# Performance work log

Hardware: AMD Instinct MI355X
Metric: run time of the kernel (lower is better)

## Reference

```python
import jax, jax.numpy as jnp
import numpy as np
from math import ceil, log2

LEVELS = 6
N = 4096
DB4 = np.array([0.23037781330885523, 0.7148465705525415, 0.6308807679295904,
                -0.02798376941698385, -0.18703481171888114, 0.030841381835986965,
                0.032883011666982945, -0.010597401784997278], dtype=np.float32)


def setup_inputs() -> dict:
    key = jax.random.key(0)
    x = jax.random.normal(key, (N, N), dtype=jnp.float32)
    # learned filter bank: scaling.repeat(levels*2, 1)
    scaling = jnp.tile(jnp.asarray(DB4), (LEVELS * 2, 1))
    return {
        "x": x,
        "scaling": scaling,
        "alpha": jnp.float32(10.0),
        "b_plus": jnp.float32(2.0),
        "b_minus": jnp.float32(1.0),
    }


def compute_wavelet(h):
    # g_k = flip(h); odd indices negated
    g = jnp.flip(h, -1)
    sign = jnp.where(jnp.arange(g.shape[-1]) % 2 == 1, -1.0, 1.0).astype(g.dtype)
    return g * sign


def convolve(x, f, transpose=False):
    # circular convolution (or correlation if transpose) along last axis via FFT,
    # exactly as torch rfft/irfft with n=input_length
    L = x.shape[-1]
    fa = jnp.fft.rfft(x, axis=-1)
    fb = jnp.fft.rfft(f, n=L)
    if transpose:
        fb = jnp.conj(fb)
    return jnp.fft.irfft(fa * fb, n=L, axis=-1)


def forward_layer(x, h):
    w = compute_wavelet(h)
    return convolve(x, w)[:, ::2], convolve(x, h)[:, ::2]


def backward_layer(d, a, h):
    w = compute_wavelet(h)
    fd = jnp.zeros((d.shape[0], d.shape[1] * 2), d.dtype).at[:, ::2].set(d)
    fa = jnp.zeros((a.shape[0], a.shape[1] * 2), a.dtype).at[:, ::2].set(a)
    return convolve(fd, w, transpose=True) + convolve(fa, h, transpose=True)


def forward2d(x, hH, hV):
    d, a = forward_layer(x, hH)
    hh, hl = forward_layer(d.T, hV)
    hh, hl = hh.T, hl.T
    lh, ll = forward_layer(a.T, hV)
    lh, ll = lh.T, ll.T
    return (hh, hl, lh), ll


def backward2d(hh, hl, lh, ll, hH, hV):
    h = backward_layer(hh.T, hl.T, hV).T
    l = backward_layer(lh.T, ll.T, hV).T
    return backward_layer(h, l, hH)


def _despawn(x, scaling, alpha, b_plus, b_minus):
    n, m = x.shape
    pn = 2 ** ceil(log2(n)) - n
    pm = 2 ** ceil(log2(m)) - m
    xp = jnp.pad(x, ((0, pn), (0, pm)), mode="edge") if (pn or pm) else x

    approx = xp
    coeffs = []
    for lev in range(LEVELS):
        dets, approx = forward2d(approx, scaling[lev], scaling[lev + 1])
        coeffs.append(dets)

    def thr(t):
        return t * (jax.nn.sigmoid(alpha * (t - b_plus)) + jax.nn.sigmoid(-alpha * (t + b_minus)))

    filt = [tuple(thr(c) for c in tup) for tup in coeffs] + [thr(approx)]

    a = filt[-1]
    for lev in reversed(range(LEVELS)):
        hh, hl, lh = filt[lev]
        a = backward2d(hh, hl, lh, a, scaling[lev], scaling[lev + 1])

    flat = jnp.concatenate(
        [jnp.concatenate(tup, axis=-1).reshape(-1) for tup in filt[:-1]]
        + [filt[-1].reshape(-1)]
    )
    return a[:n, :m], flat


def reference(x, scaling, alpha, b_plus, b_minus):
    return _despawn(x, scaling, alpha, b_plus, b_minus)
```

## Files before the change

### kernel.cpp

```cpp
#include <hip/hip_runtime.h>


__device__ __forceinline__ float thrf(float t, float alpha, float bp, float bm) {
    float s1 = 1.0f / (1.0f + __expf(-alpha * (t - bp)));
    float s2 = 1.0f / (1.0f + __expf( alpha * (t + bm)));
    return t * (s1 + s2);
}

__device__ __forceinline__ void load_h(const float* __restrict__ filt,
                                       float (&h)[8]) {
#pragma unroll
    for (int k = 0; k < 8; ++k) h[k] = filt[k];
}

struct SMemF { float Ds[70][36]; float As[70][36]; };
struct SMemI { float Hs[64][36]; float Ls[64][36]; };

__device__ __forceinline__ void fwd_tile(
    SMemF& sm, const float* __restrict__ X, int s, int sh,
    float* __restrict__ flat, float* __restrict__ All, bool thr_ll,
    const float (&h)[8], const float (&g)[8],
    float alpha, float bp, float bm, int i0, int j0, int tid) {
    const int smk = s - 1;
    for (int idx = tid; idx < 70 * 8; idx += 256) {
        int rr = idx >> 3, q = idx & 7;
        int gr = (2 * i0 - 7 + rr) & smk;
        const float* xrow = X + (size_t)gr * s;
        int cbase = 2 * j0 - 8 + 8 * q;
        float wv[16];
#pragma unroll
        for (int m = 0; m < 4; ++m) {
            float4 t = *(const float4*)&xrow[(cbase + 4 * m) & smk];
            wv[4 * m + 0] = t.x; wv[4 * m + 1] = t.y;
            wv[4 * m + 2] = t.z; wv[4 * m + 3] = t.w;
        }
        float d[4], a[4];
#pragma unroll
        for (int e = 0; e < 4; ++e) {
            float dd = 0.f, aa = 0.f;
#pragma unroll
            for (int u = 0; u < 8; ++u) {
                float v = wv[2 * e + 1 + u];
                aa += h[7 - u] * v;
                dd += (u & 1) ? h[u] * v : -h[u] * v;
            }
            d[e] = dd; a[e] = aa;
        }
        *(float4*)&sm.Ds[rr][4 * q] = make_float4(d[0], d[1], d[2], d[3]);
        *(float4*)&sm.As[rr][4 * q] = make_float4(a[0], a[1], a[2], a[3]);
    }
    __syncthreads();
    const int j = tid & 31, iq = tid >> 5;
    {
        float Dw[14];
#pragma unroll
        for (int t = 0; t < 14; ++t) Dw[t] = sm.Ds[8 * iq + t][j];
#pragma unroll
        for (int e = 0; e < 4; ++e) {
            float hh = 0.f, hl = 0.f;
#pragma unroll
            for (int u = 0; u < 8; ++u) {
                float dv = Dw[2 * e + u];
                hl += g[7 - u] * dv;
                hh += (u & 1) ? g[u] * dv : -g[u] * dv;
            }
            int row = i0 + 4 * iq + e;
            size_t ro = (size_t)row * (3 * sh) + (j0 + j);
            flat[ro]      = thrf(hh, alpha, bp, bm);
            flat[ro + sh] = thrf(hl, alpha, bp, bm);
        }
    }
    {
        float Aw[14];
#pragma unroll
        for (int t = 0; t < 14; ++t) Aw[t] = sm.As[8 * iq + t][j];
#pragma unroll
        for (int e = 0; e < 4; ++e) {
            float lh = 0.f, ll = 0.f;
#pragma unroll
            for (int u = 0; u < 8; ++u) {
                float av = Aw[2 * e + u];
                ll += g[7 - u] * av;
                lh += (u & 1) ? g[u] * av : -g[u] * av;
            }
            int row = i0 + 4 * iq + e;
            size_t ro = (size_t)row * (3 * sh) + (j0 + j);
            flat[ro + 2 * sh] = thrf(lh, alpha, bp, bm);
            All[(size_t)row * sh + (j0 + j)] =
                thr_ll ? thrf(ll, alpha, bp, bm) : ll;
        }
    }
}

__device__ __forceinline__ void inv_tile(
    SMemI& sm, const float* __restrict__ flatl, const float* __restrict__ a,
    int astride, int sc, float* __restrict__ outp, int ostride,
    const float (&h)[8], const float (&g)[8],
    int i0, int m0, int tid) {
    const int mm = sc - 1;
    const int r0 = i0 >> 1, c0 = m0 >> 1;
    const int ds = 3 * sc;
    for (int idx = tid; idx < 16 * 36; idx += 256) {
        int q = idx / 36, jj = idx - q * 36;
        int gc = (c0 + jj) & mm;
        {
            float hv[6], lv[6];
#pragma unroll
            for (int d = 0; d < 6; ++d) {
                size_t o = (size_t)((r0 + 2 * q + d) & mm) * ds + gc;
                hv[d] = flatl[o];
                lv[d] = flatl[o + sc];
            }
            float H0 = 0.f, H1 = 0.f, H2 = 0.f, H3 = 0.f;
#pragma unroll
            for (int t = 0; t < 4; ++t) {
                float we = g[7 - 2 * t], wo = -g[6 - 2 * t];
                float he = g[2 * t],     ho = g[2 * t + 1];
                H0 += we * hv[t]     + he * lv[t];
                H1 += wo * hv[t + 1] + ho * lv[t + 1];
                H2 += we * hv[t + 1] + he * lv[t + 1];
                H3 += wo * hv[t + 2] + ho * lv[t + 2];
            }
            sm.Hs[4 * q + 0][jj] = H0; sm.Hs[4 * q + 1][jj] = H1;
            sm.Hs[4 * q + 2][jj] = H2; sm.Hs[4 * q + 3][jj] = H3;
        }
        {
            float gv[6], av[6];
#pragma unroll
            for (int d = 0; d < 6; ++d) {
                int grr = (r0 + 2 * q + d) & mm;
                gv[d] = flatl[(size_t)grr * ds + 2 * sc + gc];
                av[d] = a[(size_t)grr * astride + gc];
            }
            float L0 = 0.f, L1 = 0.f, L2 = 0.f, L3 = 0.f;
#pragma unroll
            for (int t = 0; t < 4; ++t) {
                float we = g[7 - 2 * t], wo = -g[6 - 2 * t];
                float he = g[2 * t],     ho = g[2 * t + 1];
                L0 += we * gv[t]     + he * av[t];
                L1 += wo * gv[t + 1] + ho * av[t + 1];
                L2 += we * gv[t + 1] + he * av[t + 1];
                L3 += wo * gv[t + 2] + ho * av[t + 2];
            }
            sm.Ls[4 * q + 0][jj] = L0; sm.Ls[4 * q + 1][jj] = L1;
            sm.Ls[4 * q + 2][jj] = L2; sm.Ls[4 * q + 3][jj] = L3;
        }
    }
    __syncthreads();
    for (int idx = tid; idx < 64 * 16; idx += 256) {
        int i = idx >> 4, p = idx & 15;
        const float2* hp = (const float2*)&sm.Hs[i][2 * p];
        const float2* lp = (const float2*)&sm.Ls[i][2 * p];
        float2 hA = hp[0], hB = hp[1], hC = hp[2];
        float2 lA = lp[0], lB = lp[1], lC = lp[2];
        float Hw[6] = {hA.x, hA.y, hB.x, hB.y, hC.x, hC.y};
        float Lw[6] = {lA.x, lA.y, lB.x, lB.y, lC.x, lC.y};
        float o0 = 0.f, o1 = 0.f, o2 = 0.f, o3 = 0.f;
#pragma unroll
        for (int t = 0; t < 4; ++t) {
            float we = h[7 - 2 * t], wo = -h[6 - 2 * t];
            float he = h[2 * t],     ho = h[2 * t + 1];
            o0 += we * Hw[t]     + he * Lw[t];
            o1 += wo * Hw[t + 1] + ho * Lw[t + 1];
            o2 += we * Hw[t + 1] + he * Lw[t + 1];
            o3 += wo * Hw[t + 2] + ho * Lw[t + 2];
        }
        *(float4*)&outp[(size_t)(i0 + i) * ostride + (m0 + 4 * p)] =
            make_float4(o0, o1, o2, o3);
    }
}

__global__ __launch_bounds__(256, 8) void fwd_fused(
    const float* __restrict__ X, int s, int sh,
    float* __restrict__ flat, float* __restrict__ All, int thr_ll,
    const float* __restrict__ filt_row, const float* __restrict__ filt_col,
    const float* __restrict__ ap, const float* __restrict__ bpp,
    const float* __restrict__ bmp) {
    __shared__ SMemF smem;
    float h[8], g[8];
    load_h(filt_row, h);
    load_h(filt_col, g);
    const float alpha = *ap, bp = *bpp, bm = *bmp;
    fwd_tile(smem, X, s, sh, flat, All, thr_ll != 0, h, g,
             alpha, bp, bm, blockIdx.y * 32, blockIdx.x * 32, threadIdx.x);
}

__global__ __launch_bounds__(256, 8) void inv_fused(
    const float* __restrict__ flatl, const float* __restrict__ a, int astride,
    int sc, float* __restrict__ outp, int ostride,
    const float* __restrict__ filt_col, const float* __restrict__ filt_row) {
    __shared__ SMemI smem;
    float h[8], g[8];
    load_h(filt_row, h);
    load_h(filt_col, g);
    inv_tile(smem, flatl, a, astride, sc, outp, ostride, h, g,
             blockIdx.y * 64, blockIdx.x * 64, threadIdx.x);
}

extern "C" void kernel_launch(void* const* d_in, const int* in_sizes, int n_in,
                              void* d_out, int out_size, void* d_ws, size_t ws_size,
                              hipStream_t stream) {
    const float* x    = (const float*)d_in[0];
    const float* scal = (const float*)d_in[1];
    const float* ap   = (const float*)d_in[2];
    const float* bp   = (const float*)d_in[3];
    const float* bm   = (const float*)d_in[4];
    float* out = (float*)d_out;
    float* ws  = (float*)d_ws;

    const int N = 4096;
    float* recon = out;
    float* flat  = out + 16777216;
    static const size_t Aoff[7]    = {0, 0, 4194304, 5242880, 5505024, 5570560, 5586944};
    static const size_t flatOff[6] = {0, 12582912, 15728640, 16515072, 16711680, 16760832};
    const size_t finalOff = 16773120;
    float* P0 = ws + 5591040;
    float* P1 = ws + 5591040 + 4194304;

    dim3 blk(256);

    const float* src = x;
    for (int lev = 0; lev < 6; ++lev) {
        int s = N >> lev, sh = s >> 1;
        dim3 g(sh / 32, sh / 32);
        float* All = (lev < 5) ? (ws + Aoff[lev + 1]) : (flat + finalOff);
        fwd_fused<<<g, blk, 0, stream>>>(src, s, sh, flat + flatOff[lev], All,
                                         (lev == 5) ? 1 : 0,
                                         scal + lev * 8, scal + (lev + 1) * 8,
                                         ap, bp, bm);
        src = ws + Aoff[lev + 1];
    }

    const float* a_in = flat + finalOff;
    for (int lev = 5; lev >= 0; --lev) {
        int sc = N >> (lev + 1), r = 2 * sc;
        float* outp = (lev == 0) ? recon : ((lev & 1) ? P1 : P0);
        dim3 g(r / 64, r / 64);
        inv_fused<<<g, blk, 0, stream>>>(flat + flatOff[lev], a_in, sc,
                                         sc, outp, r,
                                         scal + (lev + 1) * 8, scal + lev * 8);
        a_in = outp;
    }
}
```

Measured before the change: 287.7 us.

## Merge small middle wavelet levels into one persistent kernel with atomic barriers

Replaces the eight launches for forward levels 2-5 and inverse levels 5-2 with a single persistent kernel. Tiles are handed out by an atomic work counter, and a completion counter acts as a cross-level barrier. Only blocks on XCC 0 do work, so the spin-waiting stays within one die's L2. The second forward kernel resets the counters beforehand. This removes launch overhead and tail idle time on the tiny levels, at the cost of running those levels on a fraction of the GPU and relying on spin-waits.

```diff
diff --git a/kernel.cpp b/kernel.cpp
--- a/kernel.cpp
+++ b/kernel.cpp
@@ -15,6 +15,7 @@
 
 struct SMemF { float Ds[70][36]; float As[70][36]; };
 struct SMemI { float Hs[64][36]; float Ls[64][36]; };
+union SMem { SMemF f; SMemI i; };
 
 __device__ __forceinline__ void fwd_tile(
     SMemF& sm, const float* __restrict__ X, int s, int sh,
@@ -175,7 +176,7 @@
     float* __restrict__ flat, float* __restrict__ All, int thr_ll,
     const float* __restrict__ filt_row, const float* __restrict__ filt_col,
     const float* __restrict__ ap, const float* __restrict__ bpp,
-    const float* __restrict__ bmp) {
+    const float* __restrict__ bmp, unsigned* bar_reset) {
     __shared__ SMemF smem;
     float h[8], g[8];
     load_h(filt_row, h);
@@ -183,6 +184,8 @@
     const float alpha = *ap, bp = *bpp, bm = *bmp;
     fwd_tile(smem, X, s, sh, flat, All, thr_ll != 0, h, g,
              alpha, bp, bm, blockIdx.y * 32, blockIdx.x * 32, threadIdx.x);
+    if (bar_reset && blockIdx.x == 0 && blockIdx.y == 0 && threadIdx.x < 16)
+        bar_reset[threadIdx.x * 32] = 0u;
 }
 
 __global__ __launch_bounds__(256, 8) void inv_fused(
@@ -197,6 +200,84 @@
              blockIdx.y * 64, blockIdx.x * 64, threadIdx.x);
 }
 
+__global__ __launch_bounds__(256, 8) void core_mid(
+    const float* __restrict__ scal, const float* __restrict__ ap,
+    const float* __restrict__ bpp, const float* __restrict__ bmp,
+    float* __restrict__ out, float* __restrict__ ws, unsigned* __restrict__ bar) {
+    unsigned xcc;
+    asm volatile("s_getreg_b32 %0, hwreg(HW_REG_XCC_ID, 0, 32)" : "=s"(xcc));
+    if (xcc != 0u) return;
+    __shared__ SMem smem;
+    __shared__ int curt;
+    const int tid = threadIdx.x;
+    const float alpha = *ap, bp = *bpp, bm = *bmp;
+    const int N = 4096;
+    float* flat = out + 16777216;
+    const size_t Aoff[7]    = {0, 0, 4194304, 5242880, 5505024, 5570560, 5586944};
+    const size_t flatOff[6] = {0, 12582912, 15728640, 16515072, 16711680, 16760832};
+    const size_t finalOff = 16773120;
+    float* P0 = ws + 5591040;
+    float* P1 = ws + 5591040 + 4194304;
+
+    const float* a_in = flat + finalOff;
+    int prevNp = 0;
+
+    for (int p = 0; p < 8; ++p) {
+        const int lev = (p < 4) ? (2 + p) : (9 - p);
+        const int nt  = N >> (lev + 6);
+        const int Np  = nt * nt;
+
+        if (p > 0) {
+            if (tid == 0) {
+                while (__hip_atomic_load(&bar[256 + (p - 1) * 32], __ATOMIC_RELAXED,
+                                         __HIP_MEMORY_SCOPE_AGENT) < (unsigned)prevNp) {
+                    __builtin_amdgcn_s_sleep(1);
+                }
+            }
+            __syncthreads();
+        }
+
+        float h[8], g[8];
+        load_h(scal + lev * 8, h);
+        load_h(scal + (lev + 1) * 8, g);
+        unsigned cnt = 0;
+
+        if (p < 4) {
+            const int s = N >> lev, sh = s >> 1;
+            const float* src = ws + Aoff[lev];
+            float* All = (lev < 5) ? (ws + Aoff[lev + 1]) : (flat + finalOff);
+            for (;;) {
+                __syncthreads();
+                if (tid == 0) curt = (int)atomicAdd(&bar[p * 32], 1u);
+                __syncthreads();
+                const int t = curt;
+                if (t >= Np) break;
+                fwd_tile(smem.f, src, s, sh, flat + flatOff[lev], All, lev == 5,
+                         h, g, alpha, bp, bm, (t / nt) * 32, (t % nt) * 32, tid);
+                ++cnt;
+            }
+        } else {
+            const int sc = N >> (lev + 1), r = 2 * sc;
+            float* outp = (lev & 1) ? P1 : P0;
+            for (;;) {
+                __syncthreads();
+                if (tid == 0) curt = (int)atomicAdd(&bar[p * 32], 1u);
+                __syncthreads();
+                const int t = curt;
+                if (t >= Np) break;
+                inv_tile(smem.i, flat + flatOff[lev], a_in, sc, sc, outp, r,
+                         h, g, (t / nt) * 64, (t % nt) * 64, tid);
+                ++cnt;
+            }
+            a_in = outp;
+        }
+
+        __syncthreads();
+        if (tid == 0 && cnt) atomicAdd(&bar[256 + p * 32], cnt);
+        prevNp = Np;
+    }
+}
+
 extern "C" void kernel_launch(void* const* d_in, const int* in_sizes, int n_in,
                               void* d_out, int out_size, void* d_ws, size_t ws_size,
                               hipStream_t stream) {
@@ -208,37 +289,29 @@
     float* out = (float*)d_out;
     float* ws  = (float*)d_ws;
 
-    const int N = 4096;
     float* recon = out;
     float* flat  = out + 16777216;
     static const size_t Aoff[7]    = {0, 0, 4194304, 5242880, 5505024, 5570560, 5586944};
     static const size_t flatOff[6] = {0, 12582912, 15728640, 16515072, 16711680, 16760832};
-    const size_t finalOff = 16773120;
     float* P0 = ws + 5591040;
     float* P1 = ws + 5591040 + 4194304;
+    unsigned* bar = (unsigned*)(ws + 14680064);
 
     dim3 blk(256);
 
-    const float* src = x;
-    for (int lev = 0; lev < 6; ++lev) {
-        int s = N >> lev, sh = s >> 1;
-        dim3 g(sh / 32, sh / 32);
-        float* All = (lev < 5) ? (ws + Aoff[lev + 1]) : (flat + finalOff);
-        fwd_fused<<<g, blk, 0, stream>>>(src, s, sh, flat + flatOff[lev], All,
-                                         (lev == 5) ? 1 : 0,
-                                         scal + lev * 8, scal + (lev + 1) * 8,
-                                         ap, bp, bm);
-        src = ws + Aoff[lev + 1];
-    }
-
-    const float* a_in = flat + finalOff;
-    for (int lev = 5; lev >= 0; --lev) {
-        int sc = N >> (lev + 1), r = 2 * sc;
-        float* outp = (lev == 0) ? recon : ((lev & 1) ? P1 : P0);
-        dim3 g(r / 64, r / 64);
-        inv_fused<<<g, blk, 0, stream>>>(flat + flatOff[lev], a_in, sc,
-                                         sc, outp, r,
-                                         scal + (lev + 1) * 8, scal + lev * 8);
-        a_in = outp;
-    }
-}
+    fwd_fused<<<dim3(64, 64), blk, 0, stream>>>(
+        x, 4096, 2048, flat + flatOff[0], ws + Aoff[1], 0,
+        scal, scal + 8, ap, bp, bm, (unsigned*)nullptr);
+
+    fwd_fused<<<dim3(32, 32), blk, 0, stream>>>(
+        ws + Aoff[1], 2048, 1024, flat + flatOff[1], ws + Aoff[2], 0,
+        scal + 8, scal + 16, ap, bp, bm, bar);
+
+    core_mid<<<dim3(2048), blk, 0, stream>>>(scal, ap, bp, bm, out, ws, bar);
+
+    inv_fused<<<dim3(32, 32), blk, 0, stream>>>(
+        flat + flatOff[1], P0, 1024, 1024, P1, 2048, scal + 16, scal + 8);
+
+    inv_fused<<<dim3(64, 64), blk, 0, stream>>>(
+        flat + flatOff[0], P1, 2048, 2048, recon, 4096, scal + 8, scal);
+}
```

Measured after the change: 361.5 us. 1.26x slower.
